# Optimization experiments

Measured on AMD Instinct MI355X. Metric: run time of the kernel, lower is better.

The kernel has to match this reference:

```python
import jax, jax.numpy as jnp
import numpy as np

B, S, D = 8, 2048, 512
DK = 64  # attention_dim

def setup_inputs() -> dict:
    key = jax.random.key(0)
    k0, k1, k2, k3 = jax.random.split(key, 4)
    inputs = jax.random.normal(k0, (B, S, D), dtype=jnp.float32)
    # add_weight initializer='random_normal' -> stddev 0.05 in keras
    W_q = jax.random.normal(k1, (D, DK), dtype=jnp.float32) * 0.05
    W_k = jax.random.normal(k2, (D, DK), dtype=jnp.float32) * 0.05
    W_v = jax.random.normal(k3, (D, DK), dtype=jnp.float32) * 0.05
    return {"inputs": inputs, "W_q": W_q, "W_k": W_k, "W_v": W_v}

def reference(inputs, W_q, W_k, W_v):
    # QKV projections: [B,S,D] @ [D,DK] -> [B,S,DK]
    q = jnp.einsum('bsd,dk->bsk', inputs, W_q)
    k = jnp.einsum('bsd,dk->bsk', inputs, W_k)
    v = jnp.einsum('bsd,dk->bsk', inputs, W_v)
    scale = 1.0 / jnp.sqrt(jnp.asarray(DK, dtype=q.dtype))
    scores = jnp.einsum('bqk,bsk->bqs', q, k) * scale  # [B,S,S]
    weights = jax.nn.softmax(scores, axis=-1)
    attended = jnp.einsum('bqs,bsk->bqk', weights, v)  # [B,S,DK]
    return attended, weights
```

## Files before the change

### kernel.cpp

```cpp
#include <hip/hip_runtime.h>


typedef __bf16 bf16x8 __attribute__((ext_vector_type(8)));
typedef float f32x4 __attribute__((ext_vector_type(4)));

__device__ __forceinline__ short f2bf(float f) {
    unsigned u = __builtin_bit_cast(unsigned, f);
    u = (u + 0x7fffu + ((u >> 16) & 1u)) >> 16;
    return (short)u;
}
__device__ __forceinline__ float bf2f(short h) {
    unsigned u = ((unsigned)(unsigned short)h) << 16;
    return __builtin_bit_cast(float, u);
}
__device__ __forceinline__ bf16x8 ldfrag(const short* p) {
    return *reinterpret_cast<const bf16x8*>(p);
}
__device__ __forceinline__ f32x4 mfma16(bf16x8 a, bf16x8 b, f32x4 c) {
    return __builtin_amdgcn_mfma_f32_16x16x32_bf16(a, b, c, 0, 0, 0);
}

__global__ void wtrans_kernel(const float* __restrict__ Wq,
                              const float* __restrict__ Wk,
                              const float* __restrict__ Wv,
                              short* __restrict__ wt_hi,
                              short* __restrict__ wt_lo) {
    int idx = blockIdx.x * 256 + threadIdx.x;
    int k = idx & 511;
    int n = (idx >> 9) & 63;
    int m = idx >> 15;
    const float* W = (m == 0) ? Wq : (m == 1) ? Wk : Wv;
    float w = W[k * 64 + n];
    short hi = f2bf(w);
    wt_hi[idx] = hi;
    if (m < 2) wt_lo[idx] = f2bf(w - bf2f(hi));
}

__global__ __launch_bounds__(256) void qkv_kernel(
    const float* __restrict__ x,
    const short* __restrict__ wt_hi, const short* __restrict__ wt_lo,
    short* __restrict__ Qg, short* __restrict__ Kg, short* __restrict__ VTg) {
  __shared__ __align__(16) short Ah[32 * 40], Al[32 * 40];
  __shared__ __align__(16) short Bqh[64 * 40], Bql[64 * 40];
  __shared__ __align__(16) short Bkh[64 * 40], Bkl[64 * 40];
  __shared__ __align__(16) short Bvh[64 * 40];
  const int t = threadIdx.x;
  const int wave = t >> 6, lane = t & 63, quad = lane >> 4, l15 = lane & 15;
  const int rg = wave & 1, ntp = wave >> 1;
  const int rbase = blockIdx.x * 32;

  f32x4 accq[2] = {}, acck[2] = {}, accv[2] = {};

  for (int k0 = 0; k0 < 512; k0 += 32) {
    {
      int row = t >> 3, off = (t & 7) << 2;
      float4 v = *(const float4*)(x + (size_t)(rbase + row) * 512 + k0 + off);
      short4 h, lo;
      h.x = f2bf(v.x); lo.x = f2bf(v.x - bf2f(h.x));
      h.y = f2bf(v.y); lo.y = f2bf(v.y - bf2f(h.y));
      h.z = f2bf(v.z); lo.z = f2bf(v.z - bf2f(h.z));
      h.w = f2bf(v.w); lo.w = f2bf(v.w - bf2f(h.w));
      *(short4*)(Ah + row * 40 + off) = h;
      *(short4*)(Al + row * 40 + off) = lo;
    }
    {
      int row = t >> 2, off = (t & 3) << 3;
      int src = row * 512 + k0 + off;
      int dst = row * 40 + off;
      *(int4*)(Bqh + dst) = *(const int4*)(wt_hi + 0 * 32768 + src);
      *(int4*)(Bkh + dst) = *(const int4*)(wt_hi + 1 * 32768 + src);
      *(int4*)(Bvh + dst) = *(const int4*)(wt_hi + 2 * 32768 + src);
      *(int4*)(Bql + dst) = *(const int4*)(wt_lo + 0 * 32768 + src);
      *(int4*)(Bkl + dst) = *(const int4*)(wt_lo + 1 * 32768 + src);
    }
    __syncthreads();
    bf16x8 ah = ldfrag(Ah + (rg * 16 + l15) * 40 + quad * 8);
    bf16x8 al = ldfrag(Al + (rg * 16 + l15) * 40 + quad * 8);
    #pragma unroll
    for (int j = 0; j < 2; j++) {
      const int nt = ntp * 2 + j;
      const int boff = (nt * 16 + l15) * 40 + quad * 8;
      bf16x8 bh = ldfrag(Bqh + boff);
      accq[j] = mfma16(ah, bh, accq[j]);
      accq[j] = mfma16(al, bh, accq[j]);
      accq[j] = mfma16(ah, ldfrag(Bql + boff), accq[j]);
      bh = ldfrag(Bkh + boff);
      acck[j] = mfma16(ah, bh, acck[j]);
      acck[j] = mfma16(al, bh, acck[j]);
      acck[j] = mfma16(ah, ldfrag(Bkl + boff), acck[j]);
      accv[j] = mfma16(ah, ldfrag(Bvh + boff), accv[j]);
    }
    __syncthreads();
  }
  #pragma unroll
  for (int j = 0; j < 2; j++) {
    const int nt = ntp * 2 + j;
    #pragma unroll
    for (int r = 0; r < 4; r++) {
      int row = rbase + rg * 16 + quad * 4 + r;
      int col = nt * 16 + l15;
      Qg[(size_t)row * 64 + col] = f2bf(accq[j][r]);
      Kg[(size_t)row * 64 + col] = f2bf(acck[j][r]);
    }
  }
  short* vt = Ah;
  #pragma unroll
  for (int j = 0; j < 2; j++) {
    const int col = (ntp * 2 + j) * 16 + l15;
    short4 p;
    p.x = f2bf(accv[j][0]); p.y = f2bf(accv[j][1]);
    p.z = f2bf(accv[j][2]); p.w = f2bf(accv[j][3]);
    *(short4*)(vt + col * 40 + rg * 16 + quad * 4) = p;
  }
  __syncthreads();
  {
    const int bidx = rbase >> 11;
    int c = t >> 2, ch = (t & 3) << 3;
    *(int4*)(VTg + (size_t)bidx * 131072 + (size_t)c * 2048 + (rbase & 2047) + ch) =
        *(const int4*)(vt + c * 40 + ch);
  }
}

__device__ __forceinline__ void loadK8(bf16x8 (&kf)[8], const short* Kb,
                                       int s0, int half, int l15, int quad) {
  #pragma unroll
  for (int nt2 = 0; nt2 < 4; nt2++) {
    const short* kp =
        Kb + (size_t)(s0 + (half * 4 + nt2) * 16 + l15) * 64 + quad * 8;
    kf[nt2 * 2] = ldfrag(kp);
    kf[nt2 * 2 + 1] = ldfrag(kp + 32);
  }
}

__device__ __forceinline__ void qkexp8(const bf16x8 (&kf)[8], bf16x8 aq0,
                                       bf16x8 aq1, float sc2, float C0,
                                       float (&l)[4]) {
  #pragma unroll
  for (int nt2 = 0; nt2 < 4; nt2++) {
    f32x4 c = {};
    c = mfma16(kf[nt2 * 2], aq0, c);
    c = mfma16(kf[nt2 * 2 + 1], aq1, c);
    #pragma unroll
    for (int r = 0; r < 4; r++) l[r] += exp2f(c[r] * sc2 - C0);
  }
}

__global__ __launch_bounds__(256) void attn_kernel(
    const short* __restrict__ Qg, const short* __restrict__ Kg,
    const short* __restrict__ VTg,
    float* __restrict__ att_out, float* __restrict__ w_out) {
  __shared__ __align__(16) short Plds[4 * 2 * 16 * 72];
  __shared__ float Lb[4][16];
  __shared__ float Ob[32 * 68];
  const int t = threadIdx.x;
  const int wave = t >> 6, lane = t & 63, quad = lane >> 4, l15 = lane & 15;
  const int rg = wave & 1, half = wave >> 1;
  const int b = blockIdx.x;
  const int qbase = blockIdx.y * 32;
  const float sc2 = 0.125f * 1.44269504088896340736f;
  const float C0 = 16.0f;

  const short* Kb = Kg + (size_t)b * 2048 * 64;
  const short* Vb = VTg + (size_t)b * 131072;
  const short* qp =
      Qg + (size_t)(b * 2048 + qbase + rg * 16 + l15) * 64 + quad * 8;
  const bf16x8 aq0 = ldfrag(qp);
  const bf16x8 aq1 = ldfrag(qp + 32);

  float l[4] = {0.f, 0.f, 0.f, 0.f};
  {
    bf16x8 kfA[8], kfB[8];
    loadK8(kfA, Kb, 0, half, l15, quad);
    for (int s0 = 0; s0 < 2048; s0 += 256) {
      loadK8(kfB, Kb, s0 + 128, half, l15, quad);
      qkexp8(kfA, aq0, aq1, sc2, C0, l);
      loadK8(kfA, Kb, (s0 + 256) & 2047, half, l15, quad);
      qkexp8(kfB, aq0, aq1, sc2, C0, l);
    }
  }
  float ls = (l[0] + l[1]) + (l[2] + l[3]);
  ls += __shfl_xor(ls, 16);
  ls += __shfl_xor(ls, 32);
  if (lane < 16) Lb[wave][lane] = ls;
  __syncthreads();
  const float invl = 1.0f / (Lb[wave][l15] + Lb[wave ^ 2][l15]);

  f32x4 acc[4] = {};
  float* wrow =
      w_out + ((size_t)(b * 2048 + qbase + rg * 16 + l15)) * 2048 + half * 64;
  short* plw = Plds + wave * 2 * (16 * 72) + l15 * 72;
  bf16x8 kf[8];
  loadK8(kf, Kb, 0, half, l15, quad);
  for (int s0 = 0; s0 < 2048; s0 += 128) {
    short* pl = plw + ((s0 >> 7) & 1) * (16 * 72);
    bf16x8 vf[8];
    #pragma unroll
    for (int ks2 = 0; ks2 < 2; ks2++)
      #pragma unroll
      for (int nc = 0; nc < 4; nc++)
        vf[ks2 * 4 + nc] = ldfrag(Vb + (size_t)(nc * 16 + l15) * 2048 + s0 +
                                  half * 64 + ks2 * 32 + quad * 8);
    f32x4 cc[4];
    #pragma unroll
    for (int nt2 = 0; nt2 < 4; nt2++) {
      f32x4 c = {};
      c = mfma16(kf[nt2 * 2], aq0, c);
      c = mfma16(kf[nt2 * 2 + 1], aq1, c);
      cc[nt2] = c;
    }
    loadK8(kf, Kb, (s0 + 128) & 2047, half, l15, quad);
    #pragma unroll
    for (int nt2 = 0; nt2 < 4; nt2++) {
      f32x4 w;
      #pragma unroll
      for (int r = 0; r < 4; r++) w[r] = exp2f(cc[nt2][r] * sc2 - C0) * invl;
      *(f32x4*)(wrow + s0 + nt2 * 16 + quad * 4) = w;
      short4 pb;
      pb.x = f2bf(w[0]); pb.y = f2bf(w[1]);
      pb.z = f2bf(w[2]); pb.w = f2bf(w[3]);
      *(short4*)(pl + nt2 * 16 + quad * 4) = pb;
    }
    asm volatile("s_waitcnt lgkmcnt(0)" ::: "memory");
    #pragma unroll
    for (int ks2 = 0; ks2 < 2; ks2++) {
      bf16x8 ap = ldfrag(pl + ks2 * 32 + quad * 8);
      #pragma unroll
      for (int nc = 0; nc < 4; nc++)
        acc[nc] = mfma16(ap, vf[ks2 * 4 + nc], acc[nc]);
    }
  }
  if (half == 1) {
    #pragma unroll
    for (int nc = 0; nc < 4; nc++)
      #pragma unroll
      for (int r = 0; r < 4; r++)
        Ob[(rg * 16 + quad * 4 + r) * 68 + nc * 16 + l15] = acc[nc][r];
  }
  __syncthreads();
  if (half == 0) {
    #pragma unroll
    for (int nc = 0; nc < 4; nc++)
      #pragma unroll
      for (int r = 0; r < 4; r++) {
        int row = rg * 16 + quad * 4 + r;
        att_out[((size_t)(b * 2048 + qbase + row)) * 64 + nc * 16 + l15] =
            acc[nc][r] + Ob[row * 68 + nc * 16 + l15];
      }
  }
}

extern "C" void kernel_launch(void* const* d_in, const int* in_sizes, int n_in,
                              void* d_out, int out_size, void* d_ws, size_t ws_size,
                              hipStream_t stream) {
  const float* x  = (const float*)d_in[0];
  const float* Wq = (const float*)d_in[1];
  const float* Wk = (const float*)d_in[2];
  const float* Wv = (const float*)d_in[3];

  char* ws = (char*)d_ws;
  short* wt_hi = (short*)(ws + 0);
  short* wt_lo = (short*)(ws + 196608);
  short* Qg    = (short*)(ws + 327680);
  short* Kg    = (short*)(ws + 327680 + 2097152);
  short* VTg   = (short*)(ws + 327680 + 4194304);

  float* att  = (float*)d_out;
  float* wout = att + (size_t)8 * 2048 * 64;

  hipLaunchKernelGGL(wtrans_kernel, dim3(384), dim3(256), 0, stream,
                     Wq, Wk, Wv, wt_hi, wt_lo);
  hipLaunchKernelGGL(qkv_kernel, dim3(512), dim3(256), 0, stream,
                     x, wt_hi, wt_lo, Qg, Kg, VTg);
  hipLaunchKernelGGL(attn_kernel, dim3(8, 64), dim3(256), 0, stream,
                     Qg, Kg, VTg, att, wout);
}
```

Measured before the change: 267.0 us.

## Split attention over key chunks with partial sums and separate weights pass

Result: slower. 275.6 us (+3.2%).

```diff
diff --git a/kernel.cpp b/kernel.cpp
--- a/kernel.cpp
+++ b/kernel.cpp
@@ -121,100 +121,59 @@
   }
 }
 
-__device__ __forceinline__ void loadK8(bf16x8 (&kf)[8], const short* Kb,
-                                       int s0, int half, int l15, int quad) {
-  #pragma unroll
-  for (int nt2 = 0; nt2 < 4; nt2++) {
-    const short* kp =
-        Kb + (size_t)(s0 + (half * 4 + nt2) * 16 + l15) * 64 + quad * 8;
-    kf[nt2 * 2] = ldfrag(kp);
-    kf[nt2 * 2 + 1] = ldfrag(kp + 32);
-  }
-}
-
-__device__ __forceinline__ void qkexp8(const bf16x8 (&kf)[8], bf16x8 aq0,
-                                       bf16x8 aq1, float sc2, float C0,
-                                       float (&l)[4]) {
-  #pragma unroll
-  for (int nt2 = 0; nt2 < 4; nt2++) {
-    f32x4 c = {};
-    c = mfma16(kf[nt2 * 2], aq0, c);
-    c = mfma16(kf[nt2 * 2 + 1], aq1, c);
-    #pragma unroll
-    for (int r = 0; r < 4; r++) l[r] += exp2f(c[r] * sc2 - C0);
-  }
-}
-
-__global__ __launch_bounds__(256) void attn_kernel(
+__global__ __launch_bounds__(256) void pass1_kernel(
     const short* __restrict__ Qg, const short* __restrict__ Kg,
     const short* __restrict__ VTg,
-    float* __restrict__ att_out, float* __restrict__ w_out) {
+    float* __restrict__ Lpart, float* __restrict__ Opart) {
   __shared__ __align__(16) short Plds[4 * 2 * 16 * 72];
   __shared__ float Lb[4][16];
   __shared__ float Ob[32 * 68];
   const int t = threadIdx.x;
   const int wave = t >> 6, lane = t & 63, quad = lane >> 4, l15 = lane & 15;
   const int rg = wave & 1, half = wave >> 1;
-  const int b = blockIdx.x;
-  const int qbase = blockIdx.y * 32;
+  const int b = blockIdx.x, qbase = blockIdx.y * 32, sc = blockIdx.z;
   const float sc2 = 0.125f * 1.44269504088896340736f;
   const float C0 = 16.0f;
 
-  const short* Kb = Kg + (size_t)b * 2048 * 64;
+  const short* Kb = Kg + (size_t)b * 131072;
   const short* Vb = VTg + (size_t)b * 131072;
   const short* qp =
       Qg + (size_t)(b * 2048 + qbase + rg * 16 + l15) * 64 + quad * 8;
   const bf16x8 aq0 = ldfrag(qp);
   const bf16x8 aq1 = ldfrag(qp + 32);
 
-  float l[4] = {0.f, 0.f, 0.f, 0.f};
-  {
-    bf16x8 kfA[8], kfB[8];
-    loadK8(kfA, Kb, 0, half, l15, quad);
-    for (int s0 = 0; s0 < 2048; s0 += 256) {
-      loadK8(kfB, Kb, s0 + 128, half, l15, quad);
-      qkexp8(kfA, aq0, aq1, sc2, C0, l);
-      loadK8(kfA, Kb, (s0 + 256) & 2047, half, l15, quad);
-      qkexp8(kfB, aq0, aq1, sc2, C0, l);
-    }
-  }
-  float ls = (l[0] + l[1]) + (l[2] + l[3]);
-  ls += __shfl_xor(ls, 16);
-  ls += __shfl_xor(ls, 32);
-  if (lane < 16) Lb[wave][lane] = ls;
-  __syncthreads();
-  const float invl = 1.0f / (Lb[wave][l15] + Lb[wave ^ 2][l15]);
-
+  float lsum = 0.f;
   f32x4 acc[4] = {};
-  float* wrow =
-      w_out + ((size_t)(b * 2048 + qbase + rg * 16 + l15)) * 2048 + half * 64;
-  short* plw = Plds + wave * 2 * (16 * 72) + l15 * 72;
-  bf16x8 kf[8];
-  loadK8(kf, Kb, 0, half, l15, quad);
-  for (int s0 = 0; s0 < 2048; s0 += 128) {
+  short* plw = Plds + wave * (2 * 16 * 72) + l15 * 72;
+
+  for (int s0 = 0; s0 < 512; s0 += 128) {
+    const int sg = sc * 512 + s0;
     short* pl = plw + ((s0 >> 7) & 1) * (16 * 72);
+    bf16x8 kf[8];
+    #pragma unroll
+    for (int nt2 = 0; nt2 < 4; nt2++) {
+      int off = (sg + (half * 4 + nt2) * 16 + l15) * 64 + quad * 8;
+      kf[nt2 * 2] = ldfrag(Kb + off);
+      kf[nt2 * 2 + 1] = ldfrag(Kb + off + 32);
+    }
     bf16x8 vf[8];
     #pragma unroll
     for (int ks2 = 0; ks2 < 2; ks2++)
       #pragma unroll
       for (int nc = 0; nc < 4; nc++)
-        vf[ks2 * 4 + nc] = ldfrag(Vb + (size_t)(nc * 16 + l15) * 2048 + s0 +
+        vf[ks2 * 4 + nc] = ldfrag(Vb + (nc * 16 + l15) * 2048 + sg +
                                   half * 64 + ks2 * 32 + quad * 8);
-    f32x4 cc[4];
     #pragma unroll
     for (int nt2 = 0; nt2 < 4; nt2++) {
       f32x4 c = {};
       c = mfma16(kf[nt2 * 2], aq0, c);
       c = mfma16(kf[nt2 * 2 + 1], aq1, c);
-      cc[nt2] = c;
-    }
-    loadK8(kf, Kb, (s0 + 128) & 2047, half, l15, quad);
-    #pragma unroll
-    for (int nt2 = 0; nt2 < 4; nt2++) {
       f32x4 w;
       #pragma unroll
-      for (int r = 0; r < 4; r++) w[r] = exp2f(cc[nt2][r] * sc2 - C0) * invl;
-      *(f32x4*)(wrow + s0 + nt2 * 16 + quad * 4) = w;
+      for (int r = 0; r < 4; r++) {
+        w[r] = exp2f(c[r] * sc2 - C0);
+        lsum += w[r];
+      }
       short4 pb;
       pb.x = f2bf(w[0]); pb.y = f2bf(w[1]);
       pb.z = f2bf(w[2]); pb.w = f2bf(w[3]);
@@ -229,6 +188,13 @@
         acc[nc] = mfma16(ap, vf[ks2 * 4 + nc], acc[nc]);
     }
   }
+  lsum += __shfl_xor(lsum, 16);
+  lsum += __shfl_xor(lsum, 32);
+  if (lane < 16) Lb[wave][lane] = lsum;
+  __syncthreads();
+  if (half == 0 && lane < 16)
+    Lpart[(size_t)sc * 16384 + b * 2048 + qbase + rg * 16 + lane] =
+        Lb[wave][lane] + Lb[wave ^ 2][lane];
   if (half == 1) {
     #pragma unroll
     for (int nc = 0; nc < 4; nc++)
@@ -243,10 +209,72 @@
       #pragma unroll
       for (int r = 0; r < 4; r++) {
         int row = rg * 16 + quad * 4 + r;
-        att_out[((size_t)(b * 2048 + qbase + row)) * 64 + nc * 16 + l15] =
-            acc[nc][r] + Ob[row * 68 + nc * 16 + l15];
+        Opart[((size_t)sc * 16384 + b * 2048 + qbase + row) * 64 + nc * 16 +
+              l15] = acc[nc][r] + Ob[row * 68 + nc * 16 + l15];
       }
   }
+}
+
+__global__ __launch_bounds__(256) void weights_kernel(
+    const short* __restrict__ Qg, const short* __restrict__ Kg,
+    const float* __restrict__ Lpart, float* __restrict__ w_out) {
+  const int t = threadIdx.x;
+  const int wave = t >> 6, lane = t & 63, quad = lane >> 4, l15 = lane & 15;
+  const int rg = wave & 1, half = wave >> 1;
+  const int b = blockIdx.x, qbase = blockIdx.y * 32, sc = blockIdx.z;
+  const float sc2 = 0.125f * 1.44269504088896340736f;
+  const float C0 = 16.0f;
+
+  const short* Kb = Kg + (size_t)b * 131072;
+  const int qrow = b * 2048 + qbase + rg * 16 + l15;
+  const short* qp = Qg + (size_t)qrow * 64 + quad * 8;
+  const bf16x8 aq0 = ldfrag(qp);
+  const bf16x8 aq1 = ldfrag(qp + 32);
+
+  const float l = Lpart[qrow] + Lpart[16384 + qrow] + Lpart[32768 + qrow] +
+                  Lpart[49152 + qrow];
+  const float invl = 1.0f / l;
+  float* wrow = w_out + (size_t)qrow * 2048 + sc * 512 + half * 64;
+
+  for (int s0 = 0; s0 < 512; s0 += 128) {
+    const int sg = sc * 512 + s0;
+    bf16x8 kf[8];
+    #pragma unroll
+    for (int nt2 = 0; nt2 < 4; nt2++) {
+      int off = (sg + (half * 4 + nt2) * 16 + l15) * 64 + quad * 8;
+      kf[nt2 * 2] = ldfrag(Kb + off);
+      kf[nt2 * 2 + 1] = ldfrag(Kb + off + 32);
+    }
+    #pragma unroll
+    for (int nt2 = 0; nt2 < 4; nt2++) {
+      f32x4 c = {};
+      c = mfma16(kf[nt2 * 2], aq0, c);
+      c = mfma16(kf[nt2 * 2 + 1], aq1, c);
+      f32x4 w;
+      #pragma unroll
+      for (int r = 0; r < 4; r++) w[r] = exp2f(c[r] * sc2 - C0) * invl;
+      *(f32x4*)(wrow + s0 + nt2 * 16 + quad * 4) = w;
+    }
+  }
+}
+
+__global__ __launch_bounds__(256) void finalize_kernel(
+    const float* __restrict__ Lpart, const float* __restrict__ Opart,
+    float* __restrict__ att_out) {
+  int idx = blockIdx.x * 256 + threadIdx.x;
+  int row = idx >> 4, c4 = (idx & 15) << 2;
+  float l = Lpart[row] + Lpart[16384 + row] + Lpart[32768 + row] +
+            Lpart[49152 + row];
+  float inv = 1.0f / l;
+  size_t base = (size_t)row * 64 + c4;
+  f32x4 o = *(const f32x4*)(Opart + base);
+  o += *(const f32x4*)(Opart + 1048576 + base);
+  o += *(const f32x4*)(Opart + 2097152 + base);
+  o += *(const f32x4*)(Opart + 3145728 + base);
+  f32x4 r;
+  #pragma unroll
+  for (int i = 0; i < 4; i++) r[i] = o[i] * inv;
+  *(f32x4*)(att_out + base) = r;
 }
 
 extern "C" void kernel_launch(void* const* d_in, const int* in_sizes, int n_in,
@@ -263,6 +291,8 @@
   short* Qg    = (short*)(ws + 327680);
   short* Kg    = (short*)(ws + 327680 + 2097152);
   short* VTg   = (short*)(ws + 327680 + 4194304);
+  float* Lpart = (float*)(ws + 6619136);
+  float* Opart = (float*)(ws + 6881280);
 
   float* att  = (float*)d_out;
   float* wout = att + (size_t)8 * 2048 * 64;
@@ -271,6 +301,10 @@
                      Wq, Wk, Wv, wt_hi, wt_lo);
   hipLaunchKernelGGL(qkv_kernel, dim3(512), dim3(256), 0, stream,
                      x, wt_hi, wt_lo, Qg, Kg, VTg);
-  hipLaunchKernelGGL(attn_kernel, dim3(8, 64), dim3(256), 0, stream,
-                     Qg, Kg, VTg, att, wout);
-}
+  hipLaunchKernelGGL(pass1_kernel, dim3(8, 64, 4), dim3(256), 0, stream,
+                     Qg, Kg, VTg, Lpart, Opart);
+  hipLaunchKernelGGL(weights_kernel, dim3(8, 64, 4), dim3(256), 0, stream,
+                     Qg, Kg, Lpart, wout);
+  hipLaunchKernelGGL(finalize_kernel, dim3(1024), dim3(256), 0, stream,
+                     Lpart, Opart, att);
+}
```

## Stage K and V tiles through shared memory instead of per-wave global loads

Applied to the files above, without the earlier changes.

Result: slower. 293.1 us (+9.8%).

```diff
diff --git a/kernel.cpp b/kernel.cpp
--- a/kernel.cpp
+++ b/kernel.cpp
@@ -121,27 +121,36 @@
   }
 }
 
-__device__ __forceinline__ void loadK8(bf16x8 (&kf)[8], const short* Kb,
-                                       int s0, int half, int l15, int quad) {
-  #pragma unroll
-  for (int nt2 = 0; nt2 < 4; nt2++) {
-    const short* kp =
-        Kb + (size_t)(s0 + (half * 4 + nt2) * 16 + l15) * 64 + quad * 8;
-    kf[nt2 * 2] = ldfrag(kp);
-    kf[nt2 * 2 + 1] = ldfrag(kp + 32);
-  }
-}
-
-__device__ __forceinline__ void qkexp8(const bf16x8 (&kf)[8], bf16x8 aq0,
-                                       bf16x8 aq1, float sc2, float C0,
-                                       float (&l)[4]) {
-  #pragma unroll
-  for (int nt2 = 0; nt2 < 4; nt2++) {
-    f32x4 c = {};
-    c = mfma16(kf[nt2 * 2], aq0, c);
-    c = mfma16(kf[nt2 * 2 + 1], aq1, c);
-    #pragma unroll
-    for (int r = 0; r < 4; r++) l[r] += exp2f(c[r] * sc2 - C0);
+__device__ __forceinline__ void load_k_regs(int4 (&kr)[4], const short* Kb,
+                                            int s0, int t) {
+  #pragma unroll
+  for (int i = 0; i < 4; i++) {
+    int c = t + i * 256, row = c >> 3, off = (c & 7) << 3;
+    kr[i] = *(const int4*)(Kb + (size_t)(s0 + row) * 64 + off);
+  }
+}
+__device__ __forceinline__ void store_k_lds(const int4 (&kr)[4], short* Ks,
+                                            int t) {
+  #pragma unroll
+  for (int i = 0; i < 4; i++) {
+    int c = t + i * 256, row = c >> 3, off = (c & 7) << 3;
+    *(int4*)(Ks + row * 72 + off) = kr[i];
+  }
+}
+__device__ __forceinline__ void load_v_regs(int4 (&vr)[4], const short* Vb,
+                                            int s0, int t) {
+  #pragma unroll
+  for (int i = 0; i < 4; i++) {
+    int c = t + i * 256, row = c >> 4, off = (c & 15) << 3;
+    vr[i] = *(const int4*)(Vb + (size_t)row * 2048 + s0 + off);
+  }
+}
+__device__ __forceinline__ void store_v_lds(const int4 (&vr)[4], short* Vs,
+                                            int t) {
+  #pragma unroll
+  for (int i = 0; i < 4; i++) {
+    int c = t + i * 256, row = c >> 4, off = (c & 15) << 3;
+    *(int4*)(Vs + row * 136 + off) = vr[i];
   }
 }
 
@@ -149,7 +158,9 @@
     const short* __restrict__ Qg, const short* __restrict__ Kg,
     const short* __restrict__ VTg,
     float* __restrict__ att_out, float* __restrict__ w_out) {
-  __shared__ __align__(16) short Plds[4 * 2 * 16 * 72];
+  __shared__ __align__(16) short Ks[128 * 72];
+  __shared__ __align__(16) short Vs[64 * 136];
+  __shared__ __align__(16) short Plds[4 * 16 * 72];
   __shared__ float Lb[4][16];
   __shared__ float Ob[32 * 68];
   const int t = threadIdx.x;
@@ -160,55 +171,67 @@
   const float sc2 = 0.125f * 1.44269504088896340736f;
   const float C0 = 16.0f;
 
-  const short* Kb = Kg + (size_t)b * 2048 * 64;
+  const short* Kb = Kg + (size_t)b * 131072;
   const short* Vb = VTg + (size_t)b * 131072;
   const short* qp =
       Qg + (size_t)(b * 2048 + qbase + rg * 16 + l15) * 64 + quad * 8;
   const bf16x8 aq0 = ldfrag(qp);
   const bf16x8 aq1 = ldfrag(qp + 32);
 
-  float l[4] = {0.f, 0.f, 0.f, 0.f};
-  {
-    bf16x8 kfA[8], kfB[8];
-    loadK8(kfA, Kb, 0, half, l15, quad);
-    for (int s0 = 0; s0 < 2048; s0 += 256) {
-      loadK8(kfB, Kb, s0 + 128, half, l15, quad);
-      qkexp8(kfA, aq0, aq1, sc2, C0, l);
-      loadK8(kfA, Kb, (s0 + 256) & 2047, half, l15, quad);
-      qkexp8(kfB, aq0, aq1, sc2, C0, l);
-    }
-  }
-  float ls = (l[0] + l[1]) + (l[2] + l[3]);
-  ls += __shfl_xor(ls, 16);
-  ls += __shfl_xor(ls, 32);
-  if (lane < 16) Lb[wave][lane] = ls;
+  int4 kr[4], vr[4];
+
+  float lsum = 0.f;
+  load_k_regs(kr, Kb, 0, t);
+  store_k_lds(kr, Ks, t);
+  __syncthreads();
+  for (int s0 = 0; s0 < 2048; s0 += 128) {
+    const bool more = s0 + 128 < 2048;
+    if (more) load_k_regs(kr, Kb, s0 + 128, t);
+    #pragma unroll
+    for (int nt2 = 0; nt2 < 4; nt2++) {
+      const int koff = ((half * 4 + nt2) * 16 + l15) * 72 + quad * 8;
+      f32x4 c = {};
+      c = mfma16(ldfrag(Ks + koff), aq0, c);
+      c = mfma16(ldfrag(Ks + koff + 32), aq1, c);
+      #pragma unroll
+      for (int r = 0; r < 4; r++) lsum += exp2f(c[r] * sc2 - C0);
+    }
+    __syncthreads();
+    if (more) store_k_lds(kr, Ks, t);
+    __syncthreads();
+  }
+  lsum += __shfl_xor(lsum, 16);
+  lsum += __shfl_xor(lsum, 32);
+  if (lane < 16) Lb[wave][lane] = lsum;
   __syncthreads();
   const float invl = 1.0f / (Lb[wave][l15] + Lb[wave ^ 2][l15]);
 
   f32x4 acc[4] = {};
   float* wrow =
       w_out + ((size_t)(b * 2048 + qbase + rg * 16 + l15)) * 2048 + half * 64;
-  short* plw = Plds + wave * 2 * (16 * 72) + l15 * 72;
-  bf16x8 kf[8];
-  loadK8(kf, Kb, 0, half, l15, quad);
+  short* pl = Plds + wave * (16 * 72) + l15 * 72;
+
+  load_k_regs(kr, Kb, 0, t);
+  load_v_regs(vr, Vb, 0, t);
+  __syncthreads();
+  store_k_lds(kr, Ks, t);
+  store_v_lds(vr, Vs, t);
+  __syncthreads();
   for (int s0 = 0; s0 < 2048; s0 += 128) {
-    short* pl = plw + ((s0 >> 7) & 1) * (16 * 72);
-    bf16x8 vf[8];
-    #pragma unroll
-    for (int ks2 = 0; ks2 < 2; ks2++)
-      #pragma unroll
-      for (int nc = 0; nc < 4; nc++)
-        vf[ks2 * 4 + nc] = ldfrag(Vb + (size_t)(nc * 16 + l15) * 2048 + s0 +
-                                  half * 64 + ks2 * 32 + quad * 8);
+    const bool more = s0 + 128 < 2048;
+    if (more) {
+      load_k_regs(kr, Kb, s0 + 128, t);
+      load_v_regs(vr, Vb, s0 + 128, t);
+    }
     f32x4 cc[4];
     #pragma unroll
     for (int nt2 = 0; nt2 < 4; nt2++) {
+      const int koff = ((half * 4 + nt2) * 16 + l15) * 72 + quad * 8;
       f32x4 c = {};
-      c = mfma16(kf[nt2 * 2], aq0, c);
-      c = mfma16(kf[nt2 * 2 + 1], aq1, c);
+      c = mfma16(ldfrag(Ks + koff), aq0, c);
+      c = mfma16(ldfrag(Ks + koff + 32), aq1, c);
       cc[nt2] = c;
     }
-    loadK8(kf, Kb, (s0 + 128) & 2047, half, l15, quad);
     #pragma unroll
     for (int nt2 = 0; nt2 < 4; nt2++) {
       f32x4 w;
@@ -226,8 +249,16 @@
       bf16x8 ap = ldfrag(pl + ks2 * 32 + quad * 8);
       #pragma unroll
       for (int nc = 0; nc < 4; nc++)
-        acc[nc] = mfma16(ap, vf[ks2 * 4 + nc], acc[nc]);
-    }
+        acc[nc] = mfma16(
+            ap, ldfrag(Vs + (nc * 16 + l15) * 136 + half * 64 + ks2 * 32 + quad * 8),
+            acc[nc]);
+    }
+    __syncthreads();
+    if (more) {
+      store_k_lds(kr, Ks, t);
+      store_v_lds(vr, Vs, t);
+    }
+    __syncthreads();
   }
   if (half == 1) {
     #pragma unroll
```
